# Optimization experiments

Hardware: AMD Instinct MI355X
Metric: run time of the kernel (lower is better)

## Reference

```python
import jax, jax.numpy as jnp
import numpy as np

H = 512          # hidden_size
FP = 256         # feature_padding
E = 512          # embedding_dim
NF = 768         # number of feature embeddings; num_features = NF + FP
L, B = 512, 32   # max_len, batch


def setup_inputs() -> dict:
    key = jax.random.key(0)
    ks = jax.random.split(key, 7)
    s = 0.02
    return {
        "feature_embeddings": jax.random.normal(ks[0], (NF, E), jnp.float32),
        "encoder_outputs": jax.random.normal(ks[1], (L, B, 2 * H), jnp.float32),
        "W_lin": jax.random.normal(ks[2], (H, 2 * H), jnp.float32) * s,   # linear_attn.weight
        "b_lin": jax.random.normal(ks[3], (H,), jnp.float32) * s,         # linear_attn.bias
        "W_feat": jax.random.normal(ks[4], (E, 2 * H), jnp.float32) * s,  # feature_attn.weight
        "b_feat": jax.random.normal(ks[5], (E,), jnp.float32) * s,        # feature_attn.bias
        "v": jax.random.normal(ks[6], (FP, H), jnp.float32) * s,          # self.v
    }


def reference(feature_embeddings, encoder_outputs, W_lin, b_lin, W_feat, b_feat, v):
    # encoder_outputs: [L, B, 2H]
    wh = jnp.einsum('lbi,hi->lbh', encoder_outputs, W_lin) + b_lin      # [L,B,H]
    vwh = jnp.einsum('fh,lbh->lbf', v, wh)                              # [L,B,FP]
    wh2 = jnp.einsum('lbi,ei->lbe', encoder_outputs, W_feat) + b_feat   # [L,B,E]
    fwh = jnp.einsum('ne,lbe->lbn', feature_embeddings, wh2)            # [L,B,NF]
    energy = jnp.concatenate([fwh, vwh], axis=-1)                       # [L,B,NF+FP]
    attn = jax.nn.softmax(energy, axis=-1)                              # softmax over features
    # attn_energies was [B, L, N]; .transpose(1,2) -> [B, N, L]
    return jnp.transpose(attn, (1, 2, 0))
```

## Files before the change

### kernel.cpp

```cpp
#include <hip/hip_runtime.h>
#include <hip/hip_bf16.h>
#include <math.h>

#define Hd   512
#define FPd  256
#define Ed   512
#define NFd  768
#define Ld   512
#define Bd   32
#define K2H  1024
#define Nd   1024
#define Md   (Ld * Bd)

typedef _Float16 f16x8  __attribute__((ext_vector_type(8)));
typedef _Float16 f16x4  __attribute__((ext_vector_type(4)));
typedef float    f32x4  __attribute__((ext_vector_type(4)));
typedef float    f32x16 __attribute__((ext_vector_type(16)));

__global__ __launch_bounds__(256)
void build_wpack(const float* __restrict__ F,
                 const float* __restrict__ Wf,
                 const float* __restrict__ V,
                 const float* __restrict__ Wl,
                 _Float16* __restrict__ Bh) {
    __shared__ float fs[32][68];
    __shared__ float ws[64][36];
    __shared__ float wtile[32][36];
    const int tid = threadIdx.x;
    const int kx  = blockIdx.x;
    const int ny  = blockIdx.y;
    const int n0  = ny * 32;
    const int kl  = tid & 31;
    const int ty  = tid >> 5;

    const float* src;  const float* wsrc;
    if (n0 < NFd) { src = F + (size_t)n0 * Ed;          wsrc = Wf; }
    else          { src = V + (size_t)(n0 - NFd) * Hd;  wsrc = Wl; }
    const float* wbase = wsrc + kx * 32;

    float acc[4];
#pragma unroll
    for (int i = 0; i < 4; i++) acc[i] = 0.f;

    for (int e0 = 0; e0 < 512; e0 += 64) {
#pragma unroll
        for (int rep = 0; rep < 2; rep++) {
            int idx = rep * 256 + tid;
            int i   = idx >> 4;
            int q   = idx & 15;
            float4 v4 = *(const float4*)(src + (size_t)i * 512 + e0 + q * 4);
            *(float4*)(&fs[i][q * 4]) = v4;
        }
#pragma unroll
        for (int rep = 0; rep < 2; rep++) {
            int idx = rep * 256 + tid;
            int e   = idx >> 3;
            int q   = idx & 7;
            float4 v4 = *(const float4*)(wbase + (size_t)(e0 + e) * K2H + q * 4);
            *(float4*)(&ws[e][q * 4]) = v4;
        }
        __syncthreads();
#pragma unroll 4
        for (int kk = 0; kk < 64; kk += 4) {
            float w0 = ws[kk + 0][kl];
            float w1 = ws[kk + 1][kl];
            float w2 = ws[kk + 2][kl];
            float w3 = ws[kk + 3][kl];
#pragma unroll
            for (int i = 0; i < 4; i++) {
                float4 f4 = *(const float4*)(&fs[ty * 4 + i][kk]);
                acc[i] += f4.x * w0 + f4.y * w1 + f4.z * w2 + f4.w * w3;
            }
        }
        __syncthreads();
    }
#pragma unroll
    for (int i = 0; i < 4; i++) wtile[ty * 4 + i][kl] = acc[i];
    __syncthreads();
    if (tid < 128) {
        const int lane = tid & 63;
        const int ksl  = tid >> 6;
        const int nl   = lane & 31;
        const int kf   = ksl * 16 + (lane >> 5) * 8;
        float w[8];
        *(float4*)(w)     = *(const float4*)(&wtile[nl][kf]);
        *(float4*)(w + 4) = *(const float4*)(&wtile[nl][kf + 4]);
        f16x8 h;
#pragma unroll
        for (int j = 0; j < 8; j++) h[j] = (_Float16)w[j];
        const size_t fo = ((size_t)((ny * 64) + (kx * 2 + ksl)) * 64 + lane) * 8;
        *(f16x8*)(Bh + fo) = h;
    }
}

__global__ __launch_bounds__(64)
void build_bias(const float* __restrict__ F, const float* __restrict__ bf,
                const float* __restrict__ V, const float* __restrict__ bl,
                float* __restrict__ bias) {
    const int n    = blockIdx.x;
    const int lane = threadIdx.x;
    const float* row; const float* bsrc;
    if (n < NFd) { row = F + (size_t)n * Ed;          bsrc = bf; }
    else         { row = V + (size_t)(n - NFd) * Hd;  bsrc = bl; }
    float a = 0.f;
#pragma unroll
    for (int rep = 0; rep < 8; rep++) {
        int e = rep * 64 + lane;
        a += row[e] * bsrc[e];
    }
#pragma unroll
    for (int off = 1; off < 64; off <<= 1) a += __shfl_xor(a, off);
    if (lane == 0) bias[n] = a;
}

__global__ __launch_bounds__(1024)
void gemm_direct(const float* __restrict__ enc,
                 const _Float16* __restrict__ Bh,
                 const float* __restrict__ bias,
                 float* __restrict__ out) {
    __shared__ char AsB[2][8192];
    __shared__ float red[16][64];
    __shared__ float redc[64];

    const int tid  = threadIdx.x;
    const int lane = tid & 63;
    const int wn   = tid >> 6;
    const int hf   = lane >> 5;
    const int l31  = lane & 31;
    const int b    = blockIdx.x >> 3;
    const int l0   = (blockIdx.x & 7) * 64;

    float bv[2];
#pragma unroll
    for (int nt = 0; nt < 2; nt++) bv[nt] = bias[wn * 64 + nt * 32 + l31];
    f32x16 acc[2][2];
#pragma unroll
    for (int ms = 0; ms < 2; ms++)
#pragma unroll
        for (int nt = 0; nt < 2; nt++)
#pragma unroll
            for (int r = 0; r < 16; r++) acc[ms][nt][r] = bv[nt];

    const int srow = tid >> 4;
    const int skf  = (tid & 15) * 4;
    const float* gA = enc + ((size_t)(l0 + srow) * Bd + b) * K2H + skf;

    const int kk_w   = skf >> 4;
    const int lh_w   = (skf & 15) >> 3;
    const int j0_w   = skf & 7;
    const int lane_w = lh_w * 32 + (srow & 31);
    const int slot_w = lane_w ^ ((lane_w >> 3) & 7) ^ kk_w;
    const uint32_t wb = (uint32_t)((srow >> 5) * 4096 + kk_w * 1024 + slot_w * 16 + j0_w * 2);

    const uint32_t rb16 = (uint32_t)((lane ^ ((lane >> 3) & 7)) << 4);

    const _Float16* Bp0 = Bh + ((size_t)(wn * 2 + 0) * 4096 + lane) * 8;
    const _Float16* Bp1 = Bh + ((size_t)(wn * 2 + 1) * 4096 + lane) * 8;

#define STAGE_CHUNK(dst, p)                                               \
    {                                                                     \
        f16x4 h_;                                                         \
        _Pragma("unroll")                                                 \
        for (int j = 0; j < 4; j++) h_[j] = (_Float16)((p)[j]);           \
        *(f16x4*)((dst) + wb) = h_;                                       \
    }

    {
        f32x4 p0 = __builtin_nontemporal_load((const f32x4*)gA);
        STAGE_CHUNK(AsB[0], p0)
    }
    f16x8 b_cur0 = *(const f16x8*)(Bp0);
    f16x8 b_cur1 = *(const f16x8*)(Bp1);
    f16x8 b_nx0  = *(const f16x8*)(Bp0 + 512);
    f16x8 b_nx1  = *(const f16x8*)(Bp1 + 512);

    for (int c = 0; c < 16; ++c) {
        __syncthreads();
        f32x4 pfA;
        if (c < 15) pfA = __builtin_nontemporal_load((const f32x4*)(gA + (c + 1) * 64));
        const char* hbase = AsB[c & 1];
#pragma unroll
        for (int kk = 0; kk < 4; ++kk) {
            const uint32_t ko = (uint32_t)(kk * 1024) + (rb16 ^ (uint32_t)(kk << 4));
            f16x8 a0 = *(const f16x8*)(hbase + ko);
            f16x8 a1 = *(const f16x8*)(hbase + 4096 + ko);
            const size_t t2 = (size_t)(c * 4 + kk + 2) * 512;
            f16x8 b_n20 = *(const f16x8*)(Bp0 + t2);
            f16x8 b_n21 = *(const f16x8*)(Bp1 + t2);
            __builtin_amdgcn_s_setprio(1);
            acc[0][0] = __builtin_amdgcn_mfma_f32_32x32x16_f16(a0, b_cur0, acc[0][0], 0, 0, 0);
            acc[1][0] = __builtin_amdgcn_mfma_f32_32x32x16_f16(a1, b_cur0, acc[1][0], 0, 0, 0);
            acc[0][1] = __builtin_amdgcn_mfma_f32_32x32x16_f16(a0, b_cur1, acc[0][1], 0, 0, 0);
            acc[1][1] = __builtin_amdgcn_mfma_f32_32x32x16_f16(a1, b_cur1, acc[1][1], 0, 0, 0);
            __builtin_amdgcn_s_setprio(0);
            b_cur0 = b_nx0; b_cur1 = b_nx1;
            b_nx0 = b_n20;  b_nx1 = b_n21;
        }
        if (c < 15) STAGE_CHUNK(AsB[(c + 1) & 1], pfA)
    }

#pragma unroll
    for (int ms = 0; ms < 2; ms++) {
#pragma unroll
        for (int r = 0; r < 16; r++) {
            float mx = fmaxf(acc[ms][0][r], acc[ms][1][r]);
#pragma unroll
            for (int off = 1; off < 32; off <<= 1) mx = fmaxf(mx, __shfl_xor(mx, off));
            if (l31 == r) red[wn][ms * 32 + (r & 3) + 8 * (r >> 2) + 4 * hf] = mx;
        }
    }
    __syncthreads();
    if (tid < 64) {
        float v = red[0][tid];
#pragma unroll
        for (int w = 1; w < 16; w++) v = fmaxf(v, red[w][tid]);
        redc[tid] = v;
    }
    __syncthreads();

#pragma unroll
    for (int ms = 0; ms < 2; ms++) {
#pragma unroll
        for (int r = 0; r < 16; r++) {
            const int rr = ms * 32 + (r & 3) + 8 * (r >> 2) + 4 * hf;
            const float rm = redc[rr];
            float s = 0.f;
#pragma unroll
            for (int nt = 0; nt < 2; nt++) {
                float e = __expf(acc[ms][nt][r] - rm);
                acc[ms][nt][r] = e;
                s += e;
            }
#pragma unroll
            for (int off = 1; off < 32; off <<= 1) s += __shfl_xor(s, off);
            if (l31 == r) red[wn][rr] = s;
        }
    }
    __syncthreads();
    if (tid < 64) {
        float v = 0.f;
#pragma unroll
        for (int w = 0; w < 16; w++) v += red[w][tid];
        redc[tid] = 1.0f / v;
    }
    __syncthreads();

#pragma unroll
    for (int ms = 0; ms < 2; ms++) {
        float invr[16];
#pragma unroll
        for (int r = 0; r < 16; r++)
            invr[r] = redc[ms * 32 + (r & 3) + 8 * (r >> 2) + 4 * hf];
#pragma unroll
        for (int nt = 0; nt < 2; nt++) {
            const int n = wn * 64 + nt * 32 + l31;
            float* op = out + ((size_t)b * Nd + n) * Ld + l0 + ms * 32 + hf * 4;
#pragma unroll
            for (int g = 0; g < 4; g++) {
                float4 v = make_float4(acc[ms][nt][g * 4 + 0] * invr[g * 4 + 0],
                                       acc[ms][nt][g * 4 + 1] * invr[g * 4 + 1],
                                       acc[ms][nt][g * 4 + 2] * invr[g * 4 + 2],
                                       acc[ms][nt][g * 4 + 3] * invr[g * 4 + 3]);
                *(float4*)(op + 8 * g) = v;
            }
        }
    }
}

extern "C" void kernel_launch(void* const* d_in, const int* in_sizes, int n_in,
                              void* d_out, int out_size, void* d_ws, size_t ws_size,
                              hipStream_t stream) {
    (void)in_sizes; (void)n_in; (void)out_size; (void)ws_size;

    const float* F    = (const float*)d_in[0];
    const float* enc  = (const float*)d_in[1];
    const float* Wlin = (const float*)d_in[2];
    const float* blin = (const float*)d_in[3];
    const float* Wfea = (const float*)d_in[4];
    const float* bfea = (const float*)d_in[5];
    const float* V    = (const float*)d_in[6];
    float* out = (float*)d_out;

    char* ws = (char*)d_ws;
    float*    bias = (float*)ws;
    _Float16* Bh   = (_Float16*)(ws + 0x10000);

    build_wpack<<<dim3(32, 32), 256, 0, stream>>>(F, Wfea, V, Wlin, Bh);
    build_bias<<<dim3(1024), 64, 0, stream>>>(F, bfea, V, blin, bias);
    gemm_direct<<<dim3(256), 1024, 0, stream>>>(enc, Bh, bias, out);
}
```

Baseline: 112.6 us.

## Retile fused GEMM-softmax to 32-row blocks with 512 threads and 4 N-tiles per wave

Changes the fused GEMM+softmax kernel from 256 blocks of 1024 threads (64 rows each) to 512 blocks of 512 threads (32 rows each). Each of the 8 waves now covers 128 output columns with four 32x32 MFMA tiles sharing one A fragment, instead of 16 waves covering 64 columns over two row tiles. The aim is more blocks for better CU occupancy on the 256-CU device and smaller LDS and reduction arrays. In exchange, B weights are re-read from global/L2 twice as often per output row, and the register prefetch of B fragments is removed.

```diff
diff --git a/kernel.cpp b/kernel.cpp
--- a/kernel.cpp
+++ b/kernel.cpp
@@ -113,33 +113,31 @@
     if (lane == 0) bias[n] = a;
 }
 
-__global__ __launch_bounds__(1024)
+__global__ __launch_bounds__(512, 4)
 void gemm_direct(const float* __restrict__ enc,
                  const _Float16* __restrict__ Bh,
                  const float* __restrict__ bias,
                  float* __restrict__ out) {
-    __shared__ char AsB[2][8192];
-    __shared__ float red[16][64];
-    __shared__ float redc[64];
+    __shared__ char AsB[2][4096];
+    __shared__ float red[8][32];
+    __shared__ float redc[32];
 
     const int tid  = threadIdx.x;
     const int lane = tid & 63;
     const int wn   = tid >> 6;
     const int hf   = lane >> 5;
     const int l31  = lane & 31;
-    const int b    = blockIdx.x >> 3;
-    const int l0   = (blockIdx.x & 7) * 64;
-
-    float bv[2];
-#pragma unroll
-    for (int nt = 0; nt < 2; nt++) bv[nt] = bias[wn * 64 + nt * 32 + l31];
-    f32x16 acc[2][2];
-#pragma unroll
-    for (int ms = 0; ms < 2; ms++)
-#pragma unroll
-        for (int nt = 0; nt < 2; nt++)
-#pragma unroll
-            for (int r = 0; r < 16; r++) acc[ms][nt][r] = bv[nt];
+    const int b    = blockIdx.x >> 4;
+    const int l0   = (blockIdx.x & 15) * 32;
+
+    float bv[4];
+#pragma unroll
+    for (int nt = 0; nt < 4; nt++) bv[nt] = bias[wn * 128 + nt * 32 + l31];
+    f32x16 acc[4];
+#pragma unroll
+    for (int nt = 0; nt < 4; nt++)
+#pragma unroll
+        for (int r = 0; r < 16; r++) acc[nt][r] = bv[nt];
 
     const int srow = tid >> 4;
     const int skf  = (tid & 15) * 4;
@@ -148,14 +146,16 @@
     const int kk_w   = skf >> 4;
     const int lh_w   = (skf & 15) >> 3;
     const int j0_w   = skf & 7;
-    const int lane_w = lh_w * 32 + (srow & 31);
-    const int slot_w = lane_w ^ ((lane_w >> 3) & 7) ^ kk_w;
-    const uint32_t wb = (uint32_t)((srow >> 5) * 4096 + kk_w * 1024 + slot_w * 16 + j0_w * 2);
+    const int lane_w = lh_w * 32 + srow;
+    const int slot_w = (lane_w ^ ((lane_w >> 3) & 7)) ^ kk_w;
+    const uint32_t wb = (uint32_t)(kk_w * 1024 + slot_w * 16 + j0_w * 2);
 
     const uint32_t rb16 = (uint32_t)((lane ^ ((lane >> 3) & 7)) << 4);
 
-    const _Float16* Bp0 = Bh + ((size_t)(wn * 2 + 0) * 4096 + lane) * 8;
-    const _Float16* Bp1 = Bh + ((size_t)(wn * 2 + 1) * 4096 + lane) * 8;
+    const _Float16* Bp0 = Bh + ((size_t)(wn * 4 + 0) * 4096 + lane) * 8;
+    const _Float16* Bp1 = Bh + ((size_t)(wn * 4 + 1) * 4096 + lane) * 8;
+    const _Float16* Bp2 = Bh + ((size_t)(wn * 4 + 2) * 4096 + lane) * 8;
+    const _Float16* Bp3 = Bh + ((size_t)(wn * 4 + 3) * 4096 + lane) * 8;
 
 #define STAGE_CHUNK(dst, p)                                               \
     {                                                                     \
@@ -169,10 +169,6 @@
         f32x4 p0 = __builtin_nontemporal_load((const f32x4*)gA);
         STAGE_CHUNK(AsB[0], p0)
     }
-    f16x8 b_cur0 = *(const f16x8*)(Bp0);
-    f16x8 b_cur1 = *(const f16x8*)(Bp1);
-    f16x8 b_nx0  = *(const f16x8*)(Bp0 + 512);
-    f16x8 b_nx1  = *(const f16x8*)(Bp1 + 512);
 
     for (int c = 0; c < 16; ++c) {
         __syncthreads();
@@ -183,86 +179,76 @@
         for (int kk = 0; kk < 4; ++kk) {
             const uint32_t ko = (uint32_t)(kk * 1024) + (rb16 ^ (uint32_t)(kk << 4));
             f16x8 a0 = *(const f16x8*)(hbase + ko);
-            f16x8 a1 = *(const f16x8*)(hbase + 4096 + ko);
-            const size_t t2 = (size_t)(c * 4 + kk + 2) * 512;
-            f16x8 b_n20 = *(const f16x8*)(Bp0 + t2);
-            f16x8 b_n21 = *(const f16x8*)(Bp1 + t2);
+            const size_t t = (size_t)(c * 4 + kk) * 512;
+            f16x8 b0 = *(const f16x8*)(Bp0 + t);
+            f16x8 b1 = *(const f16x8*)(Bp1 + t);
+            f16x8 b2 = *(const f16x8*)(Bp2 + t);
+            f16x8 b3 = *(const f16x8*)(Bp3 + t);
             __builtin_amdgcn_s_setprio(1);
-            acc[0][0] = __builtin_amdgcn_mfma_f32_32x32x16_f16(a0, b_cur0, acc[0][0], 0, 0, 0);
-            acc[1][0] = __builtin_amdgcn_mfma_f32_32x32x16_f16(a1, b_cur0, acc[1][0], 0, 0, 0);
-            acc[0][1] = __builtin_amdgcn_mfma_f32_32x32x16_f16(a0, b_cur1, acc[0][1], 0, 0, 0);
-            acc[1][1] = __builtin_amdgcn_mfma_f32_32x32x16_f16(a1, b_cur1, acc[1][1], 0, 0, 0);
+            acc[0] = __builtin_amdgcn_mfma_f32_32x32x16_f16(a0, b0, acc[0], 0, 0, 0);
+            acc[1] = __builtin_amdgcn_mfma_f32_32x32x16_f16(a0, b1, acc[1], 0, 0, 0);
+            acc[2] = __builtin_amdgcn_mfma_f32_32x32x16_f16(a0, b2, acc[2], 0, 0, 0);
+            acc[3] = __builtin_amdgcn_mfma_f32_32x32x16_f16(a0, b3, acc[3], 0, 0, 0);
             __builtin_amdgcn_s_setprio(0);
-            b_cur0 = b_nx0; b_cur1 = b_nx1;
-            b_nx0 = b_n20;  b_nx1 = b_n21;
         }
         if (c < 15) STAGE_CHUNK(AsB[(c + 1) & 1], pfA)
     }
 
 #pragma unroll
-    for (int ms = 0; ms < 2; ms++) {
-#pragma unroll
-        for (int r = 0; r < 16; r++) {
-            float mx = fmaxf(acc[ms][0][r], acc[ms][1][r]);
-#pragma unroll
-            for (int off = 1; off < 32; off <<= 1) mx = fmaxf(mx, __shfl_xor(mx, off));
-            if (l31 == r) red[wn][ms * 32 + (r & 3) + 8 * (r >> 2) + 4 * hf] = mx;
-        }
-    }
-    __syncthreads();
-    if (tid < 64) {
+    for (int r = 0; r < 16; r++) {
+        float mx = fmaxf(fmaxf(acc[0][r], acc[1][r]), fmaxf(acc[2][r], acc[3][r]));
+#pragma unroll
+        for (int off = 1; off < 32; off <<= 1) mx = fmaxf(mx, __shfl_xor(mx, off));
+        if (l31 == r) red[wn][(r & 3) + 8 * (r >> 2) + 4 * hf] = mx;
+    }
+    __syncthreads();
+    if (tid < 32) {
         float v = red[0][tid];
 #pragma unroll
-        for (int w = 1; w < 16; w++) v = fmaxf(v, red[w][tid]);
+        for (int w = 1; w < 8; w++) v = fmaxf(v, red[w][tid]);
         redc[tid] = v;
     }
     __syncthreads();
 
 #pragma unroll
-    for (int ms = 0; ms < 2; ms++) {
-#pragma unroll
-        for (int r = 0; r < 16; r++) {
-            const int rr = ms * 32 + (r & 3) + 8 * (r >> 2) + 4 * hf;
-            const float rm = redc[rr];
-            float s = 0.f;
-#pragma unroll
-            for (int nt = 0; nt < 2; nt++) {
-                float e = __expf(acc[ms][nt][r] - rm);
-                acc[ms][nt][r] = e;
-                s += e;
-            }
-#pragma unroll
-            for (int off = 1; off < 32; off <<= 1) s += __shfl_xor(s, off);
-            if (l31 == r) red[wn][rr] = s;
-        }
-    }
-    __syncthreads();
-    if (tid < 64) {
+    for (int r = 0; r < 16; r++) {
+        const int rr = (r & 3) + 8 * (r >> 2) + 4 * hf;
+        const float rm = redc[rr];
+        float s = 0.f;
+#pragma unroll
+        for (int nt = 0; nt < 4; nt++) {
+            float e = __expf(acc[nt][r] - rm);
+            acc[nt][r] = e;
+            s += e;
+        }
+#pragma unroll
+        for (int off = 1; off < 32; off <<= 1) s += __shfl_xor(s, off);
+        if (l31 == r) red[wn][rr] = s;
+    }
+    __syncthreads();
+    if (tid < 32) {
         float v = 0.f;
 #pragma unroll
-        for (int w = 0; w < 16; w++) v += red[w][tid];
+        for (int w = 0; w < 8; w++) v += red[w][tid];
         redc[tid] = 1.0f / v;
     }
     __syncthreads();
 
-#pragma unroll
-    for (int ms = 0; ms < 2; ms++) {
-        float invr[16];
-#pragma unroll
-        for (int r = 0; r < 16; r++)
-            invr[r] = redc[ms * 32 + (r & 3) + 8 * (r >> 2) + 4 * hf];
-#pragma unroll
-        for (int nt = 0; nt < 2; nt++) {
-            const int n = wn * 64 + nt * 32 + l31;
-            float* op = out + ((size_t)b * Nd + n) * Ld + l0 + ms * 32 + hf * 4;
-#pragma unroll
-            for (int g = 0; g < 4; g++) {
-                float4 v = make_float4(acc[ms][nt][g * 4 + 0] * invr[g * 4 + 0],
-                                       acc[ms][nt][g * 4 + 1] * invr[g * 4 + 1],
-                                       acc[ms][nt][g * 4 + 2] * invr[g * 4 + 2],
-                                       acc[ms][nt][g * 4 + 3] * invr[g * 4 + 3]);
-                *(float4*)(op + 8 * g) = v;
-            }
+    float invr[16];
+#pragma unroll
+    for (int r = 0; r < 16; r++) invr[r] = redc[(r & 3) + 8 * (r >> 2) + 4 * hf];
+
+#pragma unroll
+    for (int nt = 0; nt < 4; nt++) {
+        const int n = wn * 128 + nt * 32 + l31;
+        float* op = out + ((size_t)b * Nd + n) * Ld + l0 + hf * 4;
+#pragma unroll
+        for (int g = 0; g < 4; g++) {
+            float4 v = make_float4(acc[nt][g * 4 + 0] * invr[g * 4 + 0],
+                                   acc[nt][g * 4 + 1] * invr[g * 4 + 1],
+                                   acc[nt][g * 4 + 2] * invr[g * 4 + 2],
+                                   acc[nt][g * 4 + 3] * invr[g * 4 + 3]);
+            *(float4*)(op + 8 * g) = v;
         }
     }
 }
@@ -287,5 +273,5 @@
 
     build_wpack<<<dim3(32, 32), 256, 0, stream>>>(F, Wfea, V, Wlin, Bh);
     build_bias<<<dim3(1024), 64, 0, stream>>>(F, bfea, V, blin, bias);
-    gemm_direct<<<dim3(256), 1024, 0, stream>>>(enc, Bh, bias, out);
-}
+    gemm_direct<<<dim3(512), 512, 0, stream>>>(enc, Bh, bias, out);
+}
```

New measurement: 116.2 us. +3.2%, slower.
